# Kernel tuning notes

Hardware: AMD Instinct MI355X
Metric: run time of the kernel (lower is better)

Reference implementation:

```python
import jax, jax.numpy as jnp
import numpy as np
from jax import lax

B, CIN, H, W = 4096, 3, 64, 64
NVAR = 50

def _lin(x, w, b):
    return jax.nn.relu(x @ w + b)

def setup_inputs() -> dict:
    key = jax.random.key(0)
    ks = jax.random.split(key, 16)
    def rn(k, shape, scale=0.05):
        return jax.random.normal(k, shape, dtype=jnp.float32) * scale
    return {
        "x": jax.random.normal(ks[0], (B, CIN, H, W), dtype=jnp.float32),
        "C": jax.random.uniform(ks[1], (B, NVAR, NVAR), dtype=jnp.float32),
        "conv1_w": rn(ks[2], (32, CIN, 3, 3)), "conv1_b": jnp.zeros((32,), jnp.float32),
        "conv2_w": rn(ks[3], (64, 32, 3, 3)), "conv2_b": jnp.zeros((64,), jnp.float32),
        "enc_w": rn(ks[4], (64, 128)), "enc_b": jnp.zeros((128,), jnp.float32),
        "f1_w": rn(ks[5], (128, NVAR)), "f1_b": jnp.zeros((NVAR,), jnp.float32),
        "f2_w": rn(ks[6], (NVAR, 128)), "f2_b": jnp.zeros((128,), jnp.float32),
        "f3_w": rn(ks[7], (256, 64)), "f3_b": jnp.zeros((64,), jnp.float32),
        "f4_w": rn(ks[8], (64, 64)), "f4_b": jnp.zeros((64,), jnp.float32),
        "f5_w": rn(ks[9], (64, 64)), "f5_b": jnp.zeros((64,), jnp.float32),
        "out_w": rn(ks[10], (64, NVAR)), "out_b": jnp.zeros((NVAR,), jnp.float32),
    }

def reference(x, C, conv1_w, conv1_b, conv2_w, conv2_b, enc_w, enc_b,
              f1_w, f1_b, f2_w, f2_b, f3_w, f3_b, f4_w, f4_b, f5_w, f5_b,
              out_w, out_b):
    dn = ("NCHW", "OIHW", "NCHW")
    # Observation_Encoder_F: conv(s2)->relu->conv(s2)->relu->global mean pool->linear->relu
    h = lax.conv_general_dilated(x, conv1_w, (2, 2), ((1, 1), (1, 1)), dimension_numbers=dn)
    h = jax.nn.relu(h + conv1_b[None, :, None, None])          # [B,32,32,32]
    h = lax.conv_general_dilated(h, conv2_w, (2, 2), ((1, 1), (1, 1)), dimension_numbers=dn)
    h = jax.nn.relu(h + conv2_b[None, :, None, None])          # [B,64,16,16]
    x1 = _lin(h.mean(axis=(2, 3)), enc_w, enc_b)               # [B,128]
    x2 = _lin(x1, f1_w, f1_b)                                  # [B,V]
    # per-sample causal matrix multiply: e[b] = C[b] @ x2[b]
    e = jnp.einsum("bij,bj->bi", C, x2)                        # [B,V]
    x3 = _lin(e, f2_w, f2_b)                                   # [B,128]
    x4 = jnp.concatenate((x1, x3), axis=1)                     # [B,256]
    x5 = _lin(x4, f3_w, f3_b)
    x6 = _lin(x5, f4_w, f4_b)
    x7 = _lin(x6, f5_w, f5_b)
    return jax.nn.softmax(_lin(x7, out_w, out_b), axis=1)      # [B,V]
```

## Files before the change

### kernel.cpp

```cpp
#include <hip/hip_runtime.h>
#include <hip/hip_bf16.h>


typedef __attribute__((ext_vector_type(8)))  short short8;
typedef __attribute__((ext_vector_type(4)))  float floatx4;
typedef __attribute__((ext_vector_type(16))) float floatx16;

#define AS1 __attribute__((address_space(1)))
#define AS3 __attribute__((address_space(3)))

#define BAR_LGKM() asm volatile("s_waitcnt lgkmcnt(0)\ns_barrier" ::: "memory")
#define BAR_FULL() asm volatile("s_waitcnt vmcnt(0) lgkmcnt(0)\ns_barrier" ::: "memory")

__device__ __forceinline__ short f2bf(float f) {
    unsigned u = __float_as_uint(f);
    u += 0x7fffu + ((u >> 16) & 1u);
    return (short)(u >> 16);
}

__device__ __forceinline__ unsigned pkbf2(float a, float b) {
    float2 fp; fp.x = a; fp.y = b;
    __hip_bfloat162 bb = __float22bfloat162_rn(fp);
    return *(unsigned*)&bb;
}

#define WS_MLP_B    40960
#define WS_BIAS_B   (40960 + 115712)
#define WS_POOL_B   163840

__global__ void k_prep(const float* __restrict__ cw2, const float* __restrict__ cw1,
                       const float* __restrict__ ew,  const float* __restrict__ w1,
                       const float* __restrict__ w2,  const float* __restrict__ w3,
                       const float* __restrict__ w4,  const float* __restrict__ w5,
                       const float* __restrict__ ow,  const float* __restrict__ eb,
                       const float* __restrict__ b1,  const float* __restrict__ b2,
                       const float* __restrict__ b3,  const float* __restrict__ b4,
                       const float* __restrict__ b5,  const float* __restrict__ ob,
                       short* __restrict__ packw, float* __restrict__ biasout) {
    const int idx = blockIdx.x * 256 + threadIdx.x;
    if (idx < 18432) {
        const int ic  = idx & 31;
        const int oc  = (idx >> 5) & 63;
        const int pos = idx >> 11;
        packw[idx] = f2bf(cw2[oc * 288 + ic * 9 + pos]);
    } else if (idx < 19456) {
        const int j  = idx - 18432;
        const int k  = j & 31;
        const int oc = j >> 5;
        packw[idx] = (k < 27) ? f2bf(cw1[oc * 27 + k]) : (short)0;
    } else if (idx < 77312) {
        const int e = idx - 19456;
        short v;
        if (e < 9216)        { const int n = e / 72,  kk = e - n * 72;
            v = (kk < 64) ? f2bf(ew[kk * 128 + n]) : (short)0; }
        else if (e < 17920)  { const int r = e - 9216;  const int n = r / 136, kk = r - n * 136;
            v = (kk < 128 && n < 50) ? f2bf(w1[kk * 50 + n]) : (short)0; }
        else if (e < 27136)  { const int r = e - 17920; const int n = r / 72,  kk = r - n * 72;
            v = (kk < 50) ? f2bf(w2[kk * 128 + n]) : (short)0; }
        else if (e < 44032)  { const int r = e - 27136; const int n = r / 264, kk = r - n * 264;
            v = (kk < 256) ? f2bf(w3[kk * 64 + n]) : (short)0; }
        else if (e < 48640)  { const int r = e - 44032; const int n = r / 72,  kk = r - n * 72;
            v = (kk < 64) ? f2bf(w4[kk * 64 + n]) : (short)0; }
        else if (e < 53248)  { const int r = e - 48640; const int n = r / 72,  kk = r - n * 72;
            v = (kk < 64) ? f2bf(w5[kk * 64 + n]) : (short)0; }
        else                 { const int r = e - 53248; const int n = r / 72,  kk = r - n * 72;
            v = (kk < 64 && n < 50) ? f2bf(ow[kk * 50 + n]) : (short)0; }
        packw[20480 + e] = v;
    } else if (idx < 77888) {
        const int j = idx - 77312;
        float v;
        if (j < 128)      v = eb[j];
        else if (j < 192) v = (j - 128 < 50) ? b1[j - 128] : 0.f;
        else if (j < 320) v = b2[j - 192];
        else if (j < 384) v = b3[j - 320];
        else if (j < 448) v = b4[j - 384];
        else if (j < 512) v = b5[j - 448];
        else              v = (j - 512 < 50) ? ob[j - 512] : 0.f;
        biasout[j] = v;
    }
}

#define XS_OFF  0
#define A1_OFF  49152
#define A1STR   80
#define H1_OFF  90112
#define ROWB    2064
#define SMEM_SZ (49152 + 40960 + 66048)
#define SPB     16

__global__ __launch_bounds__(512, 2) void k_conv(
    const float* __restrict__ x,    const float* __restrict__ c1b,
    const short* __restrict__ packw, const float* __restrict__ c2b,
    float* __restrict__ pooled)
{
    __shared__ __align__(16) char smem[SMEM_SZ];
    float* xs      = (float*)(smem + XS_OFF);
    char*  a1      = smem + A1_OFF;
    char*  h1b     = smem + H1_OFF;
    float* poolbuf = (float*)(smem + A1_OFF);

    const int tid  = threadIdx.x;
    const int lane = tid & 63;
    const int w    = tid >> 6;

    const int col = lane & 31;
    const int ss  = lane >> 5;

    const int nt  = w & 1;
    const int ox2 = lane & 15;
    const int oyb = (lane >> 4) & 1;
    const int ocn = nt * 32 + col;
    const float bias2 = c2b[ocn];

    short8 z8;
    #pragma unroll
    for (int i = 0; i < 8; ++i) z8[i] = 0;

    short8 bfr[9][2];
    #pragma unroll
    for (int pos = 0; pos < 9; ++pos)
        #pragma unroll
        for (int h = 0; h < 2; ++h)
            bfr[pos][h] = *(const short8*)(packw + (pos * 64 + ocn) * 32 + h * 16 + ss * 8);

    const short* w1p = packw + 18432;
    short8 w1f[2];
    #pragma unroll
    for (int k = 0; k < 2; ++k)
        w1f[k] = *(const short8*)(w1p + col * 32 + k * 16 + ss * 8);

    float2 b1p[8];
    #pragma unroll
    for (int rp = 0; rp < 8; ++rp)
        b1p[rp] = *(const float2*)(c1b + ((rp & 1) * 2 + (rp >> 1) * 8 + 4 * ss));

    int  sbv[3][2];
    bool okx[3];
    #pragma unroll
    for (int kx = 0; kx < 3; ++kx) {
        const int ph   = (kx + 1) & 1;
        const int xh   = ox2 - (kx == 0 ? 1 : 0);
        const int slot = ph * 16 + xh;
        const int swz  = (slot >> 1) & 3;
        okx[kx] = (xh >= 0);
        #pragma unroll
        for (int h = 0; h < 2; ++h)
            sbv[kx][h] = slot * 64 + (((ss + 2 * h) ^ swz) << 4);
    }

    const int slotpx = ((col & 1) << 4) + (col >> 1);
    const int wswz   = (slotpx >> 1) & 3;
    const int wbase  = slotpx * 64 + ss * 8;

    auto prefetch_x = [&](int bb) {
        const char* g = (const char*)(x + (size_t)bb * 12288);
        #pragma unroll
        for (int i = 0; i < 6; ++i) {
            const int off = (w * 6 + i) << 10;
            __builtin_amdgcn_global_load_lds(
                (const AS1 unsigned int*)(g + off + lane * 16),
                (AS3 unsigned int*)(smem + XS_OFF + off), 16, 0, 0);
        }
    };

    auto im2col = [&](int half) {
        const int p  = tid;
        const int oy = half * 16 + (p >> 5);
        const int ox = p & 31;
        float f[32];
        #pragma unroll
        for (int ic = 0; ic < 3; ++ic) {
            #pragma unroll
            for (int ky = 0; ky < 3; ++ky) {
                const int  iy   = 2 * oy + ky - 1;
                const bool oky  = iy >= 0;
                const int  base = ic * 4096 + (oky ? iy : 0) * 64 + 2 * ox;
                const float2 p12 = *(const float2*)(xs + base);
                const float2 pm  = *(const float2*)(xs + (base >= 2 ? base - 2 : 0));
                const int k = ic * 9 + ky * 3;
                f[k + 0] = (oky && ox > 0) ? pm.y : 0.f;
                f[k + 1] = oky ? p12.x : 0.f;
                f[k + 2] = oky ? p12.y : 0.f;
            }
        }
        f[27] = 0.f; f[28] = 0.f; f[29] = 0.f; f[30] = 0.f; f[31] = 0.f;
        unsigned pk[16];
        #pragma unroll
        for (int t = 0; t < 16; ++t) pk[t] = pkbf2(f[2 * t], f[2 * t + 1]);
        uint4* dst = (uint4*)(a1 + p * A1STR);
        dst[0] = make_uint4(pk[0],  pk[1],  pk[2],  pk[3]);
        dst[1] = make_uint4(pk[4],  pk[5],  pk[6],  pk[7]);
        dst[2] = make_uint4(pk[8],  pk[9],  pk[10], pk[11]);
        dst[3] = make_uint4(pk[12], pk[13], pk[14], pk[15]);
    };

    auto conv1_mfma = [&](int half) {
        #pragma unroll
        for (int i = 0; i < 2; ++i) {
            const int t = w * 2 + i;
            const char* abase = a1 + (t * 32 + col) * A1STR + ss * 16;
            const short8 bf0 = *(const short8*)(abase);
            const short8 bf1 = *(const short8*)(abase + 32);
            floatx16 acc;
            #pragma unroll
            for (int r = 0; r < 16; ++r) acc[r] = 0.f;
            acc = __builtin_amdgcn_mfma_f32_32x32x16_bf16(w1f[0], bf0, acc, 0, 0, 0);
            acc = __builtin_amdgcn_mfma_f32_32x32x16_bf16(w1f[1], bf1, acc, 0, 0, 0);
            const int oyg = half * 16 + t;
            char* hb = h1b + oyg * ROWB + wbase;
            #pragma unroll
            for (int rp = 0; rp < 8; ++rp) {
                const unsigned u = pkbf2(fmaxf(acc[2 * rp]     + b1p[rp].x, 0.f),
                                         fmaxf(acc[2 * rp + 1] + b1p[rp].y, 0.f));
                const int off = (((rp >> 1) ^ wswz) << 4) + (rp & 1) * 4;
                *(unsigned*)(hb + off) = u;
            }
        }
    };

    prefetch_x(blockIdx.x);

    #pragma unroll 1
    for (int s = 0; s < SPB; ++s) {
        const int b = blockIdx.x + (s << 8);

        BAR_FULL();
        im2col(0);
        BAR_LGKM();
        conv1_mfma(0);
        BAR_LGKM();
        im2col(1);
        BAR_LGKM();
        if (s + 1 < SPB) prefetch_x(blockIdx.x + ((s + 1) << 8));
        conv1_mfma(1);
        BAR_LGKM();

        const int t0 = w >> 1;
        float pool = 0.f;
        floatx16 acc0, acc1;
        #pragma unroll
        for (int r = 0; r < 16; ++r) { acc0[r] = 0.f; acc1[r] = 0.f; }
        #pragma unroll
        for (int ky = 0; ky < 3; ++ky) {
            #pragma unroll
            for (int kx = 0; kx < 3; ++kx) {
                const int  iy0 = t0 * 4 + oyb * 2 + ky - 1;
                const bool ok0 = okx[kx] && (iy0 >= 0);
                const bool ok1 = okx[kx];
                const int  ba0 = iy0 * ROWB;
                const int  ba1 = ba0 + 16 * ROWB;
                #pragma unroll
                for (int h = 0; h < 2; ++h) {
                    const int so = sbv[kx][h];
                    short8 a0v = ok0 ? *(const short8*)(h1b + ba0 + so) : z8;
                    short8 a1v = ok1 ? *(const short8*)(h1b + ba1 + so) : z8;
                    const short8 bf = bfr[ky * 3 + kx][h];
                    acc0 = __builtin_amdgcn_mfma_f32_32x32x16_bf16(a0v, bf, acc0, 0, 0, 0);
                    acc1 = __builtin_amdgcn_mfma_f32_32x32x16_bf16(a1v, bf, acc1, 0, 0, 0);
                }
            }
        }
        #pragma unroll
        for (int r = 0; r < 16; ++r) {
            pool += fmaxf(acc0[r] + bias2, 0.f);
            pool += fmaxf(acc1[r] + bias2, 0.f);
        }
        pool += __shfl_xor(pool, 32, 64);
        if (lane < 32) poolbuf[w * 32 + lane] = pool;
        BAR_LGKM();
        if (tid < 64) {
            const int g = tid >> 5, c = tid & 31;
            pooled[(size_t)b * 64 + tid] =
                (poolbuf[(g    ) * 32 + c] + poolbuf[(g + 2) * 32 + c] +
                 poolbuf[(g + 4) * 32 + c] + poolbuf[(g + 6) * 32 + c]) * (1.f / 256.f);
        }
    }
}

#define ML_BIAS_B 115712
#define ML_P_SH   59392
#define ML_A_SH   60544
#define ML_B_SH   64768
#define ML_Z_F    34496
#define ML_SMEM   142336

__global__ __launch_bounds__(256, 1) void k_mlp(
    const char* __restrict__ wsblk,
    const float* __restrict__ pooled, const float* __restrict__ C,
    float* __restrict__ out)
{
    __shared__ __align__(16) char smem[ML_SMEM];
    short*       Sw   = (short*)smem;
    const short* S    = (const short*)smem;
    const float* Bias = (const float*)(smem + ML_BIAS_B);
    float*       Zf   = (float*)smem;

    const int tid    = threadIdx.x;
    const int lane   = tid & 63;
    const int w      = tid >> 6;
    const int n16    = lane & 15;
    const int q      = lane >> 4;
    const int tile16 = blockIdx.x * 16;

    #pragma unroll
    for (int i = 0; i < 29; ++i) {
        const int off = i * 4096 + w * 1024;
        __builtin_amdgcn_global_load_lds(
            (const AS1 unsigned int*)(wsblk + off + lane * 16),
            (AS3 unsigned int*)(smem + off), 16, 0, 0);
    }
    {
        const float4 pv = *(const float4*)(pooled + tile16 * 64 + tid * 4);
        const int s = tid >> 4, k = (tid & 15) * 4;
        uint2 u;
        u.x = pkbf2(pv.x, pv.y);
        u.y = pkbf2(pv.z, pv.w);
        *(uint2*)(Sw + ML_P_SH + s * 72 + k) = u;
    }
    BAR_FULL();

    auto layer = [&](int inOff, int inPitch, int K, int wOff, int nTiles,
                     int biasOff, int outOff, bool isOut) {
        #pragma unroll
        for (int nt = w; nt < nTiles; nt += 4) {
            floatx4 acc;
            acc[0] = 0.f; acc[1] = 0.f; acc[2] = 0.f; acc[3] = 0.f;
            const int kp = K + 8;
            #pragma unroll
            for (int kc = 0; kc < 8; ++kc) {
                if (kc * 32 >= K) break;
                const short8 aF = *(const short8*)(S + inOff + n16 * inPitch + kc * 32 + q * 8);
                const short8 bF = *(const short8*)(S + wOff + (nt * 16 + n16) * kp + kc * 32 + q * 8);
                acc = __builtin_amdgcn_mfma_f32_16x16x32_bf16(aF, bF, acc, 0, 0, 0);
            }
            const int   n  = nt * 16 + n16;
            const float bv = Bias[biasOff + n];
            #pragma unroll
            for (int r = 0; r < 4; ++r) {
                const int   m = q * 4 + r;
                const float v = fmaxf(acc[r] + bv, 0.f);
                if (isOut) Zf[ML_Z_F + m * 68 + n] = (n < 50) ? v : -1e30f;
                else       Sw[outOff + m * 264 + n] = f2bf(v);
            }
        }
    };

    layer(ML_P_SH, 72, 64, 0, 8, 0, ML_A_SH, false);
    BAR_LGKM();
    layer(ML_A_SH, 264, 128, 9216, 4, 128, ML_B_SH, false);
    BAR_LGKM();

    #pragma unroll
    for (int r = 0; r < 4; ++r) {
        const int item = tid + r * 256;
        if (item < 800) {
            const int s = (item * 1311) >> 16;
            const int i = item - s * 50;
            const float* Cp = C + (size_t)(tile16 + s) * 2500 + i * 50;
            float e = 0.f;
            #pragma unroll
            for (int j2 = 0; j2 < 25; ++j2) {
                const float2   cc = *(const float2*)(Cp + 2 * j2);
                const unsigned u  = *(const unsigned*)(S + ML_B_SH + s * 264 + 2 * j2);
                e += cc.x * __uint_as_float(u << 16)
                   + cc.y * __uint_as_float(u & 0xffff0000u);
            }
            Sw[ML_B_SH + s * 264 + 64 + i] = f2bf(e);
        }
    }
    if ((tid & 15) < 14)
        Sw[ML_B_SH + (tid >> 4) * 264 + 64 + 50 + (tid & 15)] = 0;
    BAR_LGKM();

    layer(ML_B_SH + 64, 264, 64, 17920, 8, 192, ML_A_SH + 128, false);
    BAR_LGKM();
    layer(ML_A_SH, 264, 256, 27136, 4, 320, ML_B_SH, false);
    BAR_LGKM();
    layer(ML_B_SH, 264, 64, 44032, 4, 384, ML_B_SH + 64, false);
    BAR_LGKM();
    layer(ML_B_SH + 64, 264, 64, 48640, 4, 448, ML_B_SH + 128, false);
    BAR_LGKM();
    layer(ML_B_SH + 128, 264, 64, 53248, 4, 512, 0, true);
    BAR_LGKM();

    {
        const int s = tid >> 4, g = tid & 15;
        const float4 zv = *(const float4*)(Zf + ML_Z_F + s * 68 + g * 4);
        float m = fmaxf(fmaxf(zv.x, zv.y), fmaxf(zv.z, zv.w));
        #pragma unroll
        for (int o = 8; o > 0; o >>= 1) m = fmaxf(m, __shfl_xor(m, o, 16));
        float4 p;
        p.x = __expf(zv.x - m); p.y = __expf(zv.y - m);
        p.z = __expf(zv.z - m); p.w = __expf(zv.w - m);
        float sum = p.x + p.y + p.z + p.w;
        #pragma unroll
        for (int o = 8; o > 0; o >>= 1) sum += __shfl_xor(sum, o, 16);
        const float inv = 1.f / sum;
        float* po = out + (size_t)(tile16 + s) * 50 + g * 4;
        const int j = g * 4;
        if (j     < 50) po[0] = p.x * inv;
        if (j + 1 < 50) po[1] = p.y * inv;
        if (j + 2 < 50) po[2] = p.z * inv;
        if (j + 3 < 50) po[3] = p.w * inv;
    }
}

extern "C" void kernel_launch(void* const* d_in, const int* in_sizes, int n_in,
                              void* d_out, int out_size, void* d_ws, size_t ws_size,
                              hipStream_t stream) {
    (void)in_sizes; (void)n_in; (void)out_size; (void)ws_size;
    const float* x   = (const float*)d_in[0];
    const float* Cm  = (const float*)d_in[1];
    const float* c1w = (const float*)d_in[2];
    const float* c1b = (const float*)d_in[3];
    const float* c2w = (const float*)d_in[4];
    const float* c2b = (const float*)d_in[5];
    const float* ew  = (const float*)d_in[6];
    const float* ebv = (const float*)d_in[7];
    const float* f1w = (const float*)d_in[8];
    const float* f1b = (const float*)d_in[9];
    const float* f2w = (const float*)d_in[10];
    const float* f2b = (const float*)d_in[11];
    const float* f3w = (const float*)d_in[12];
    const float* f3b = (const float*)d_in[13];
    const float* f4w = (const float*)d_in[14];
    const float* f4b = (const float*)d_in[15];
    const float* f5w = (const float*)d_in[16];
    const float* f5b = (const float*)d_in[17];
    const float* ow  = (const float*)d_in[18];
    const float* ob  = (const float*)d_in[19];

    short* packw   = (short*)d_ws;
    float* biasout = (float*)((char*)d_ws + WS_BIAS_B);
    float* pooled  = (float*)((char*)d_ws + WS_POOL_B);
    const char* wsblk = (const char*)d_ws + WS_MLP_B;
    float* out     = (float*)d_out;

    hipLaunchKernelGGL(k_prep, dim3(305), dim3(256), 0, stream,
                       c2w, c1w, ew, f1w, f2w, f3w, f4w, f5w, ow,
                       ebv, f1b, f2b, f3b, f4b, f5b, ob, packw, biasout);
    hipLaunchKernelGGL(k_conv, dim3(256), dim3(512), 0, stream,
                       x, c1b, packw, c2b, pooled);
    hipLaunchKernelGGL(k_mlp,  dim3(256), dim3(256), 0, stream,
                       wsblk, pooled, Cm, out);
}
```

Measured before the change: 361.9 us.

## Split input prefetch into half-image buffers with partial vmcnt waits

The single full-image LDS staging buffer is split into two halves, one with the top rows and one with the bottom rows plus a halo row. Each half is prefetched for the next sample as soon as the current half has been consumed by im2col, and barriers use partial vmcnt waits instead of draining every load. This lets the global load of the next sample overlap more of the conv1 work and shrinks the LDS footprint for x. On the last iteration it issues a redundant reload of the same sample instead of skipping the prefetch.

```diff
diff --git a/kernel.cpp b/kernel.cpp
--- a/kernel.cpp
+++ b/kernel.cpp
@@ -11,6 +11,8 @@
 
 #define BAR_LGKM() asm volatile("s_waitcnt lgkmcnt(0)\ns_barrier" ::: "memory")
 #define BAR_FULL() asm volatile("s_waitcnt vmcnt(0) lgkmcnt(0)\ns_barrier" ::: "memory")
+#define BAR_VM4()  asm volatile("s_waitcnt vmcnt(4) lgkmcnt(0)\ns_barrier" ::: "memory")
+#define BAR_VM3()  asm volatile("s_waitcnt vmcnt(3) lgkmcnt(0)\ns_barrier" ::: "memory")
 
 __device__ __forceinline__ short f2bf(float f) {
     unsigned u = __float_as_uint(f);
@@ -80,13 +82,14 @@
     }
 }
 
-#define XS_OFF  0
-#define A1_OFF  49152
-#define A1STR   80
-#define H1_OFF  90112
-#define ROWB    2064
-#define SMEM_SZ (49152 + 40960 + 66048)
-#define SPB     16
+#define XS_OFF   0
+#define XSB_OFF  24576
+#define A1_OFF   49920
+#define A1STR    80
+#define H1_OFF   90880
+#define ROWB     2064
+#define SMEM_SZ  156928
+#define SPB      16
 
 __global__ __launch_bounds__(512, 2) void k_conv(
     const float* __restrict__ x,    const float* __restrict__ c1b,
@@ -95,6 +98,7 @@
 {
     __shared__ __align__(16) char smem[SMEM_SZ];
     float* xs      = (float*)(smem + XS_OFF);
+    float* xsb     = (float*)(smem + XSB_OFF);
     char*  a1      = smem + A1_OFF;
     char*  h1b     = smem + H1_OFF;
     float* poolbuf = (float*)(smem + A1_OFF);
@@ -152,14 +156,31 @@
     const int wswz   = (slotpx >> 1) & 3;
     const int wbase  = slotpx * 64 + ss * 8;
 
-    auto prefetch_x = [&](int bb) {
+    auto issueA = [&](int bb) {
         const char* g = (const char*)(x + (size_t)bb * 12288);
         #pragma unroll
-        for (int i = 0; i < 6; ++i) {
-            const int off = (w * 6 + i) << 10;
+        for (int i = 0; i < 3; ++i) {
+            const int idx = w * 3 + i;
+            const int ic  = idx >> 3, blk = idx & 7;
+            const int so  = ic * 16384 + blk * 1024;
+            const int dof = ic * 8192  + blk * 1024;
             __builtin_amdgcn_global_load_lds(
-                (const AS1 unsigned int*)(g + off + lane * 16),
-                (AS3 unsigned int*)(smem + XS_OFF + off), 16, 0, 0);
+                (const AS1 unsigned int*)(g + so + lane * 16),
+                (AS3 unsigned int*)(smem + XS_OFF + dof), 16, 0, 0);
+        }
+    };
+    auto issueB = [&](int bb) {
+        const char* g = (const char*)(x + (size_t)bb * 12288);
+        #pragma unroll
+        for (int i = 0; i < 4; ++i) {
+            int idx = w * 4 + i;
+            if (idx >= 27) idx -= 27;
+            const int ic = idx / 9, k = idx - ic * 9;
+            const int so  = ic * 16384 + ((k == 0) ? 7936 : 8192 + (k - 1) * 1024);
+            const int dof = ic * 8448  + ((k == 0) ? 0    : 256  + (k - 1) * 1024);
+            __builtin_amdgcn_global_load_lds(
+                (const AS1 unsigned int*)(g + so + lane * 16),
+                (AS3 unsigned int*)(smem + XSB_OFF + dof), 16, 0, 0);
         }
     };
 
@@ -167,16 +188,19 @@
         const int p  = tid;
         const int oy = half * 16 + (p >> 5);
         const int ox = p & 31;
+        const int bx = 2 * ox;
         float f[32];
         #pragma unroll
         for (int ic = 0; ic < 3; ++ic) {
             #pragma unroll
             for (int ky = 0; ky < 3; ++ky) {
-                const int  iy   = 2 * oy + ky - 1;
-                const bool oky  = iy >= 0;
-                const int  base = ic * 4096 + (oky ? iy : 0) * 64 + 2 * ox;
-                const float2 p12 = *(const float2*)(xs + base);
-                const float2 pm  = *(const float2*)(xs + (base >= 2 ? base - 2 : 0));
+                const int  iy  = 2 * oy + ky - 1;
+                const bool oky = iy >= 0;
+                const float* rowp = (half == 0)
+                    ? xs  + ic * 2048 + (oky ? iy : 0) * 64
+                    : xsb + ic * 2112 + (iy - 31) * 64;
+                const float2 p12 = *(const float2*)(rowp + bx);
+                const float2 pm  = *(const float2*)(rowp + (bx >= 2 ? bx - 2 : 0));
                 const int k = ic * 9 + ky * 3;
                 f[k + 0] = (oky && ox > 0) ? pm.y : 0.f;
                 f[k + 1] = oky ? p12.x : 0.f;
@@ -218,20 +242,23 @@
         }
     };
 
-    prefetch_x(blockIdx.x);
+    issueA(blockIdx.x);
+    issueB(blockIdx.x);
 
     #pragma unroll 1
     for (int s = 0; s < SPB; ++s) {
-        const int b = blockIdx.x + (s << 8);
-
-        BAR_FULL();
+        const int b  = blockIdx.x + (s << 8);
+        const int bn = (s + 1 < SPB) ? b + 256 : b;
+
+        BAR_VM4();
         im2col(0);
         BAR_LGKM();
+        issueA(bn);
         conv1_mfma(0);
-        BAR_LGKM();
+        BAR_VM3();
         im2col(1);
         BAR_LGKM();
-        if (s + 1 < SPB) prefetch_x(blockIdx.x + ((s + 1) << 8));
+        issueB(bn);
         conv1_mfma(1);
         BAR_LGKM();
 
```

Result: no change. 358.8 us (-0.9%).
